# Optimization experiments

Measured on AMD Instinct MI355X. Metric: run time of the kernel, lower is better.

The kernel has to match this reference:

```python
import jax, jax.numpy as jnp
import numpy as np

B, N, D = 16, 1024, 5
R_HID = 8  # radial MLP hidden width


def setup_inputs() -> dict:
    key = jax.random.key(0)
    ks = jax.random.split(key, 16)
    feats = jax.random.normal(ks[0], (B, N, D), jnp.float32)
    coors = 3.0 * jax.random.normal(ks[1], (B, N, 3), jnp.float32)
    a = jax.random.bernoulli(ks[2], 0.01, (B, N, N))
    adj_mat = a | jnp.swapaxes(a, 1, 2)
    s = 1.0 / np.sqrt(D)
    Wq = s * jax.random.normal(ks[3], (D, D), jnp.float32)
    Wk = s * jax.random.normal(ks[4], (D, D), jnp.float32)
    Wv = s * jax.random.normal(ks[5], (D, D), jnp.float32)
    Wo = s * jax.random.normal(ks[6], (D, D), jnp.float32)
    w_r1 = 0.5 * jax.random.normal(ks[7], (1, R_HID), jnp.float32)
    b_r1 = jnp.zeros((R_HID,), jnp.float32)
    w_r2 = 0.5 * jax.random.normal(ks[8], (R_HID, 1), jnp.float32)
    b_r2 = jnp.zeros((1,), jnp.float32)
    w1 = (1.0 / np.sqrt(D)) * jax.random.normal(ks[9], (D, 128), jnp.float32)
    b1 = jnp.zeros((128,), jnp.float32)
    w2 = (1.0 / np.sqrt(128.0)) * jax.random.normal(ks[10], (128, 3), jnp.float32)
    b2 = jnp.zeros((3,), jnp.float32)
    return dict(feats=feats, coors=coors, adj_mat=adj_mat, Wq=Wq, Wk=Wk, Wv=Wv,
                Wo=Wo, w_r1=w_r1, b_r1=b_r1, w_r2=w_r2, b_r2=b_r2,
                w1=w1, b1=b1, w2=w2, b2=b2)


def _se3_layer(feats, coors, neigh, Wq, Wk, Wv, Wo, w_r1, b_r1, w_r2, b_r2):
    # SE(3)-invariant sparse graph attention on degree-0 channels.
    # Attention logits = content term + radial (distance-only) bias, so the
    # scalar output is invariant to global rotations/translations of coors.
    q = jnp.einsum('bnd,de->bne', feats, Wq)
    k = jnp.einsum('bnd,de->bne', feats, Wk)
    v = jnp.einsum('bnd,de->bne', feats, Wv)
    rel = coors[:, :, None, :] - coors[:, None, :, :]        # [B,N,N,3]
    dist = jnp.sqrt(jnp.sum(rel * rel, axis=-1) + 1e-8)      # [B,N,N]
    h = jax.nn.relu(dist[..., None] * w_r1[0] + b_r1)        # [B,N,N,R_HID]
    rbias = (h @ w_r2)[..., 0] + b_r2[0]                     # [B,N,N]
    scores = jnp.einsum('bid,bjd->bij', q, k) / np.sqrt(q.shape[-1]) + rbias
    scores = jnp.where(neigh, scores, -1e9)
    attn = jax.nn.softmax(scores, axis=-1)
    agg = jnp.einsum('bij,bjd->bid', attn, v)
    return feats + jnp.einsum('bid,de->bie', agg, Wo)        # residual


def reference(feats, coors, adj_mat, Wq, Wk, Wv, Wo, w_r1, b_r1, w_r2, b_r2,
              w1, b1, w2, b2):
    a = adj_mat.astype(jnp.float32)
    # num_adj_degrees=2: attend over 1-hop and 2-hop neighbors (+ self)
    adj2 = jnp.einsum('bij,bjk->bik', a, a) > 0
    eye = jnp.eye(adj_mat.shape[1], dtype=bool)[None]
    neigh = adj_mat | adj2 | eye
    x = _se3_layer(feats, coors, neigh, Wq, Wk, Wv, Wo, w_r1, b_r1, w_r2, b_r2)
    pooled = jnp.mean(x, axis=1)                              # [B, D]
    hdn = jax.nn.relu(pooled @ w1 + b1)
    return hdn @ w2 + b2                                      # [B, 3]
```

## Files before the change

### kernel.cpp

```cpp
#include <hip/hip_runtime.h>
#include <hip/hip_bf16.h>

#define BB 16
#define NN 1024
#define DD 5
#define RH 8

typedef unsigned long long u64;
typedef unsigned int u32;
typedef __hip_bfloat16 bf16;

static __device__ __forceinline__ float tof(bf16 x) { return __bfloat162float(x); }
static __device__ __forceinline__ float ldf(const void* p, long long i, bool f) {
  return f ? ((const float*)p)[i] : tof(((const bf16*)p)[i]);
}

#define LOG2E 1.4426950408889634f
#define PACK_BLOCKS (BB * NN * 16 / 256)
#define KV_BLOCKS (BB * NN / 256)


__global__ __launch_bounds__(256) void k_pack(
    const void* __restrict__ adj, const void* __restrict__ feats,
    const void* __restrict__ coors,
    const void* __restrict__ Wk, const void* __restrict__ Wv,
    const void* __restrict__ Wo,
    u64* __restrict__ adjbits, float4* __restrict__ kvg,
    float* __restrict__ czg, int* __restrict__ gflags,
    float* __restrict__ pooled, int* __restrict__ cntr) {
  __shared__ int sNon01, sNonpair, sLow3;
  __shared__ int sCnt[4];
  __shared__ float wkL[25], wvL[25], woL[25];
  int tid = threadIdx.x;

  if (blockIdx.x >= PACK_BLOCKS) {
    int kb = blockIdx.x - PACK_BLOCKS;
    if (kb == 0) {
      if (tid < BB * DD) pooled[tid] = 0.0f;
      else if (tid < BB * DD + BB) cntr[tid - BB * DD] = 0;
    }
    {
      u32 x = ((const u32*)feats)[tid];
      u32 lo = x & 0xFFFFu;
      int e = (int)((lo >> 7) & 0xFFu);
      bool insane = !(lo == 0u || (e >= 90 && e <= 150));
      u64 m = __ballot(insane);
      if ((tid & 63) == 0) sCnt[tid >> 6] = (int)__popcll(m);
    }
    __syncthreads();
    bool f32 = (sCnt[0] + sCnt[1] + sCnt[2] + sCnt[3]) > 64;
    if (tid < 25) {
      wkL[tid] = ldf(Wk, tid, f32);
      wvL[tid] = ldf(Wv, tid, f32);
      woL[tid] = ldf(Wo, tid, f32);
    }
    if (kb == 0 && tid == 0) gflags[0] = f32 ? 1 : 0;
    __syncthreads();
    long long node = (long long)kb * 256 + tid;
    float f0 = ldf(feats, node * DD + 0, f32), f1 = ldf(feats, node * DD + 1, f32),
          f2 = ldf(feats, node * DD + 2, f32), f3 = ldf(feats, node * DD + 3, f32),
          f4 = ldf(feats, node * DD + 4, f32);
    float k[DD], tv[DD], v[DD];
    #pragma unroll
    for (int e = 0; e < DD; ++e) {
      k[e] = f0 * wkL[e] + f1 * wkL[5 + e] + f2 * wkL[10 + e] + f3 * wkL[15 + e] +
             f4 * wkL[20 + e];
      tv[e] = f0 * wvL[e] + f1 * wvL[5 + e] + f2 * wvL[10 + e] + f3 * wvL[15 + e] +
              f4 * wvL[20 + e];
    }
    #pragma unroll
    for (int e = 0; e < DD; ++e)
      v[e] = tv[0] * woL[e] + tv[1] * woL[5 + e] + tv[2] * woL[10 + e] +
             tv[3] * woL[15 + e] + tv[4] * woL[20 + e];
    float cx = ldf(coors, node * 3 + 0, f32);
    float cy = ldf(coors, node * 3 + 1, f32);
    float cz = ldf(coors, node * 3 + 2, f32);
    kvg[node * 3 + 0] = make_float4(k[0], k[1], k[2], k[3]);
    kvg[node * 3 + 1] = make_float4(k[4], v[0], v[1], v[2]);
    kvg[node * 3 + 2] = make_float4(v[3], v[4], cx, cy);
    czg[node] = cz;
    return;
  }

  if (tid == 0) { sNon01 = 0; sNonpair = 0; sLow3 = 0; }
  __syncthreads();
  {
    const u32* aw = (const u32*)adj;
    int non01 = 0, nonpair = 0, low3 = 0;
    for (int i = tid; i < 4096; i += 256) {
      u32 x = aw[i];
      u32 lo = x & 0xFFFFu, hi = x >> 16;
      non01 |= (x > 1u);
      nonpair |= !((lo == 0u || lo == 0x3F80u) && (hi == 0u || hi == 0x3F80u));
      low3 |= (lo == 0x3F80u);
    }
    if (non01) atomicOr(&sNon01, 1);
    if (nonpair) atomicOr(&sNonpair, 1);
    if (low3) atomicOr(&sLow3, 1);
  }
  __syncthreads();
  int mode;
  if (!sNon01) mode = 0;
  else if (!sNonpair) mode = sLow3 ? 2 : 3;
  else mode = 1;

  int gid = blockIdx.x * 256 + tid;
  int w = gid & 15;
  long long row = gid >> 4;
  long long base = row * NN + (long long)w * 64;
  u64 bits = 0;
  if (mode == 3) {
    const uint4* p = (const uint4*)((const float*)adj + base);
    #pragma unroll
    for (int t = 0; t < 16; ++t) {
      uint4 x = p[t];
      if (x.x << 1) bits |= 1ull << (4 * t + 0);
      if (x.y << 1) bits |= 1ull << (4 * t + 1);
      if (x.z << 1) bits |= 1ull << (4 * t + 2);
      if (x.w << 1) bits |= 1ull << (4 * t + 3);
    }
  } else if (mode == 0) {
    const uint4* p = (const uint4*)((const u32*)adj + base);
    #pragma unroll
    for (int t = 0; t < 16; ++t) {
      uint4 x = p[t];
      if (x.x) bits |= 1ull << (4 * t + 0);
      if (x.y) bits |= 1ull << (4 * t + 1);
      if (x.z) bits |= 1ull << (4 * t + 2);
      if (x.w) bits |= 1ull << (4 * t + 3);
    }
  } else if (mode == 2) {
    const uint4* p = (const uint4*)((const unsigned short*)adj + base);
    #pragma unroll
    for (int t = 0; t < 8; ++t) {
      uint4 x = p[t];
      u32 c[4] = {x.x, x.y, x.z, x.w};
      #pragma unroll
      for (int q = 0; q < 4; ++q) {
        if ((c[q] & 0x7FFFu)) bits |= 1ull << (8 * t + 2 * q + 0);
        if ((c[q] >> 16) & 0x7FFFu) bits |= 1ull << (8 * t + 2 * q + 1);
      }
    }
  } else {
    const uint4* p = (const uint4*)((const unsigned char*)adj + base);
    #pragma unroll
    for (int t = 0; t < 4; ++t) {
      uint4 x = p[t];
      u32 c[4] = {x.x, x.y, x.z, x.w};
      #pragma unroll
      for (int q = 0; q < 4; ++q)
        #pragma unroll
        for (int bb = 0; bb < 4; ++bb)
          if ((c[q] >> (8 * bb)) & 0xFFu) bits |= 1ull << (16 * t + 4 * q + bb);
    }
  }
  adjbits[gid] = bits;
}

__global__ __launch_bounds__(256) void k_attn(
    const void* __restrict__ feats, const void* __restrict__ coors,
    const void* __restrict__ Wq,
    const void* __restrict__ wr1, const void* __restrict__ br1,
    const void* __restrict__ wr2, const void* __restrict__ br2,
    const float4* __restrict__ kvg, const float* __restrict__ czg,
    const int* __restrict__ gflags, const u64* __restrict__ adjbits,
    float* __restrict__ pooled, int* __restrict__ cntr,
    const void* __restrict__ w1, const void* __restrict__ b1,
    const void* __restrict__ w2, const void* __restrict__ b2,
    float* __restrict__ out) {
  __shared__ __align__(16) float4 kvL[NN * 3];
  __shared__ float czL[NN];
  __shared__ unsigned short listL[4][NN];
  __shared__ u64 neighL[16][16];
  __shared__ float qL[16 * DD], ciL[16 * 3];
  __shared__ float wqL[25];
  __shared__ float wrL[3][RH];
  __shared__ float sConst[2];
  __shared__ int sFast, sLast;

  int bi = blockIdx.x;
  int b = bi >> 6, chunk = bi & 63;
  int tid = threadIdx.x;
  bool f32 = gflags[0] != 0;
  if (tid < 25) wqL[tid] = ldf(Wq, tid, f32);
  if (tid >= 64 && tid < 64 + RH) {
    int h = tid - 64;
    wrL[0][h] = ldf(wr1, h, f32);
    wrL[1][h] = ldf(br1, h, f32);
    wrL[2][h] = ldf(wr2, h, f32);
  }
  if (tid == 96) {
    float c = 0.0f;
    int ok = 1;
    #pragma unroll
    for (int h = 0; h < RH; ++h) {
      float w1h = ldf(wr1, h, f32);
      if (ldf(br1, h, f32) != 0.0f) ok = 0;
      if (w1h > 0.0f) c += w1h * ldf(wr2, h, f32);
    }
    sConst[0] = c * LOG2E;
    sConst[1] = ldf(br2, 0, f32) * LOG2E;
    sFast = ok;
  }
  {
    const float4* src = kvg + (size_t)b * NN * 3;
    for (int idx = tid; idx < NN * 3; idx += 256) kvL[idx] = src[idx];
    const float* csrc = czg + (size_t)b * NN;
    for (int idx = tid; idx < NN; idx += 256) czL[idx] = csrc[idx];
  }
  __syncthreads();
  int fast = sFast;
  if (tid < 16) {
    long long row = (long long)b * NN + chunk * 16 + tid;
    float f0 = ldf(feats, row * DD + 0, f32), f1 = ldf(feats, row * DD + 1, f32),
          f2 = ldf(feats, row * DD + 2, f32), f3 = ldf(feats, row * DD + 3, f32),
          f4 = ldf(feats, row * DD + 4, f32);
    float qsc = fast ? (0.4472135954999579f * LOG2E) : 0.4472135954999579f;
    #pragma unroll
    for (int e = 0; e < DD; ++e)
      qL[tid * DD + e] = (f0 * wqL[e] + f1 * wqL[5 + e] + f2 * wqL[10 + e] +
                          f3 * wqL[15 + e] + f4 * wqL[20 + e]) * qsc;
    #pragma unroll
    for (int c = 0; c < 3; ++c)
      ciL[tid * 3 + c] = ldf(coors, row * 3 + c, f32);
  }

  int g = tid >> 6, lane = tid & 63;
  int w = lane & 15, grp = lane >> 4;
  const u64* basep = adjbits + (size_t)b * NN * 16;
  for (int rr = 0; rr < 4; ++rr) {
    int il = g * 4 + rr;
    int i = chunk * 16 + il;
    u64 rw = basep[(size_t)i * 16 + w];
    unsigned short* list = listL[g];
    int cnt = 0;
    #pragma unroll
    for (int sw = 0; sw < 16; ++sw) {
      u64 bits = __shfl(rw, sw, 64);
      int mybit = (int)((bits >> lane) & 1ull);
      int pre = __popcll(bits & ((1ull << lane) - 1ull));
      if (mybit) list[cnt + pre] = (unsigned short)(sw * 64 + lane);
      cnt += __popcll(bits);
    }
    __syncthreads();
    u64 acc = rw;
    if (w == (i >> 6)) acc |= 1ull << (i & 63);
    for (int n = grp; n < cnt; n += 4) acc |= basep[(size_t)list[n] * 16 + w];
    acc |= __shfl_xor(acc, 16, 64);
    acc |= __shfl_xor(acc, 32, 64);
    if (lane < 16) neighL[il][lane] = acc;
    __syncthreads();
  }

  float q[4][DD], ci[4][3], l[4], A[4][DD];
  #pragma unroll
  for (int r = 0; r < 4; ++r) {
    #pragma unroll
    for (int e = 0; e < DD; ++e) q[r][e] = qL[(g * 4 + r) * DD + e];
    #pragma unroll
    for (int c = 0; c < 3; ++c) ci[r][c] = ciL[(g * 4 + r) * 3 + c];
    l[r] = 0.0f;
    #pragma unroll
    for (int e = 0; e < DD; ++e) A[r][e] = 0.0f;
  }
  float Cf = sConst[0], br2f = sConst[1];
  for (int it = 0; it < 16; ++it) {
    int j = it * 64 + lane;
    float4 ka = kvL[j * 3 + 0];
    float4 kb = kvL[j * 3 + 1];
    float4 kc = kvL[j * 3 + 2];
    float jx = kc.z, jy = kc.w, jz = czL[j];
    u64 nw[4];
    #pragma unroll
    for (int r = 0; r < 4; ++r) nw[r] = neighL[g * 4 + r][it];
    if (fast) {
      #pragma unroll
      for (int r = 0; r < 4; ++r) {
        float cx = jx - ci[r][0], cy = jy - ci[r][1], cz = jz - ci[r][2];
        float dist =
            __builtin_amdgcn_sqrtf(fmaf(cx, cx, fmaf(cy, cy, fmaf(cz, cz, 1e-8f))));
        float s = fmaf(q[r][0], ka.x, br2f);
        s = fmaf(q[r][1], ka.y, s);
        s = fmaf(q[r][2], ka.z, s);
        s = fmaf(q[r][3], ka.w, s);
        s = fmaf(q[r][4], kb.x, s);
        s = fmaf(Cf, dist, s);
        s = fminf(s, 126.0f);
        s = ((nw[r] >> lane) & 1ull) ? s : -150.0f;
        float p = __builtin_amdgcn_exp2f(s);
        l[r] += p;
        A[r][0] = fmaf(p, kb.y, A[r][0]);
        A[r][1] = fmaf(p, kb.z, A[r][1]);
        A[r][2] = fmaf(p, kb.w, A[r][2]);
        A[r][3] = fmaf(p, kc.x, A[r][3]);
        A[r][4] = fmaf(p, kc.y, A[r][4]);
      }
    } else {
      #pragma unroll
      for (int r = 0; r < 4; ++r) {
        float cx = jx - ci[r][0], cy = jy - ci[r][1], cz = jz - ci[r][2];
        float dist = sqrtf(fmaf(cx, cx, fmaf(cy, cy, fmaf(cz, cz, 1e-8f))));
        float rb = ldf(br2, 0, f32);
        #pragma unroll
        for (int h = 0; h < RH; ++h)
          rb += fmaxf(dist * wrL[0][h] + wrL[1][h], 0.0f) * wrL[2][h];
        float s = fmaf(q[r][0], ka.x, rb);
        s = fmaf(q[r][1], ka.y, s);
        s = fmaf(q[r][2], ka.z, s);
        s = fmaf(q[r][3], ka.w, s);
        s = fmaf(q[r][4], kb.x, s);
        s = fminf(s, 85.0f);
        s = ((nw[r] >> lane) & 1ull) ? s : -100.0f;
        float p = __expf(s);
        l[r] += p;
        A[r][0] = fmaf(p, kb.y, A[r][0]);
        A[r][1] = fmaf(p, kb.z, A[r][1]);
        A[r][2] = fmaf(p, kb.w, A[r][2]);
        A[r][3] = fmaf(p, kc.x, A[r][3]);
        A[r][4] = fmaf(p, kc.y, A[r][4]);
      }
    }
  }
  #pragma unroll
  for (int msk = 1; msk < 64; msk <<= 1) {
    #pragma unroll
    for (int r = 0; r < 4; ++r) {
      l[r] += __shfl_xor(l[r], msk, 64);
      A[r][0] += __shfl_xor(A[r][0], msk, 64);
      A[r][1] += __shfl_xor(A[r][1], msk, 64);
      A[r][2] += __shfl_xor(A[r][2], msk, 64);
      A[r][3] += __shfl_xor(A[r][3], msk, 64);
      A[r][4] += __shfl_xor(A[r][4], msk, 64);
    }
  }

  float* waveC = (float*)listL;
  if (lane == 0) {
    float cw[DD] = {0.f, 0.f, 0.f, 0.f, 0.f};
    #pragma unroll
    for (int r = 0; r < 4; ++r) {
      long long grow = (long long)b * NN + chunk * 16 + g * 4 + r;
      float inv = (l[r] > 0.0f) ? 1.0f / l[r] : 0.0f;
      #pragma unroll
      for (int e = 0; e < DD; ++e)
        cw[e] += ldf(feats, grow * DD + e, f32) + A[r][e] * inv;
    }
    #pragma unroll
    for (int e = 0; e < DD; ++e) waveC[g * DD + e] = cw[e];
  }
  __syncthreads();
  if (tid < DD) {
    float s = waveC[tid] + waveC[DD + tid] + waveC[2 * DD + tid] +
              waveC[3 * DD + tid];
    float old = atomicAdd(&pooled[b * DD + tid], s);
    asm volatile("" :: "v"(old));
  }
  __syncthreads();
  if (tid == 0) sLast = (atomicAdd(&cntr[b], 1) == 63) ? 1 : 0;
  __syncthreads();

  if (sLast) {
    float* hL = ((float*)listL) + 32;
    if (tid < DD) {
      float pv = __hip_atomic_load(&pooled[b * DD + tid], __ATOMIC_RELAXED,
                                   __HIP_MEMORY_SCOPE_AGENT);
      qL[tid] = pv * (1.0f / 1024.0f);
    }
    __syncthreads();
    if (tid < 128) {
      float acc = ldf(b1, tid, f32);
      #pragma unroll
      for (int d = 0; d < DD; ++d)
        acc = fmaf(qL[d], ldf(w1, d * 128 + tid, f32), acc);
      hL[tid] = fmaxf(acc, 0.0f);
    }
    __syncthreads();
    if (tid < 3) {
      float s = ldf(b2, tid, f32);
      for (int j = 0; j < 128; ++j)
        s = fmaf(hL[j], ldf(w2, j * 3 + tid, f32), s);
      out[b * 3 + tid] = s;
    }
  }
}

extern "C" void kernel_launch(void* const* d_in, const int* in_sizes, int n_in,
                              void* d_out, int out_size, void* d_ws, size_t ws_size,
                              hipStream_t stream) {
  const void* adj = d_in[2];
  float* out = (float*)d_out;

  char* w = (char*)d_ws;
  int* gflags = (int*)w;
  float* pooled = (float*)(w + 64);
  int* cntr = (int*)(w + 512);
  const size_t MB2 = (size_t)BB * NN * 16 * sizeof(u64);
  u64* adjbits = (u64*)(w + 1024);
  float4* kvg = (float4*)(w + 1024 + MB2);
  float* czg = (float*)(w + 1024 + MB2 + 786432);

  k_pack<<<PACK_BLOCKS + KV_BLOCKS, 256, 0, stream>>>(
      adj, d_in[0], d_in[1], d_in[4], d_in[5], d_in[6], adjbits, kvg, czg,
      gflags, pooled, cntr);
  k_attn<<<BB * 64, 256, 0, stream>>>(
      d_in[0], d_in[1], d_in[3], d_in[7], d_in[8], d_in[9], d_in[10], kvg, czg,
      gflags, adjbits, pooled, cntr, d_in[11], d_in[12], d_in[13], d_in[14],
      out);
}
```

Measured before the change: 202.2 us.

## Read per-batch K/V and coords from global instead of staging in LDS

Removes the 64 KB LDS staging of the per-batch key/value/coordinate table and has each lane load its float4 entries directly from global memory (served by L2, shared across the 64 blocks of a batch). This cuts LDS use per block to raise occupancy and drops the upfront bulk copy. The per-row __syncthreads in the neighbor-list build are also removed, since each wave uses its own list buffer, and dedicated small shared arrays replace the aliased reuse of listL. The trade-off is stride-3 float4 global loads inside the hot loop instead of LDS reads.

```diff
diff --git a/kernel.cpp b/kernel.cpp
--- a/kernel.cpp
+++ b/kernel.cpp
@@ -168,8 +168,6 @@
     const void* __restrict__ w1, const void* __restrict__ b1,
     const void* __restrict__ w2, const void* __restrict__ b2,
     float* __restrict__ out) {
-  __shared__ __align__(16) float4 kvL[NN * 3];
-  __shared__ float czL[NN];
   __shared__ unsigned short listL[4][NN];
   __shared__ u64 neighL[16][16];
   __shared__ float qL[16 * DD], ciL[16 * 3];
@@ -177,6 +175,9 @@
   __shared__ float wrL[3][RH];
   __shared__ float sConst[2];
   __shared__ int sFast, sLast;
+  __shared__ float waveC[4][DD];
+  __shared__ float pM[DD];
+  __shared__ float hL[128];
 
   int bi = blockIdx.x;
   int b = bi >> 6, chunk = bi & 63;
@@ -202,12 +203,6 @@
     sConst[1] = ldf(br2, 0, f32) * LOG2E;
     sFast = ok;
   }
-  {
-    const float4* src = kvg + (size_t)b * NN * 3;
-    for (int idx = tid; idx < NN * 3; idx += 256) kvL[idx] = src[idx];
-    const float* csrc = czg + (size_t)b * NN;
-    for (int idx = tid; idx < NN; idx += 256) czL[idx] = csrc[idx];
-  }
   __syncthreads();
   int fast = sFast;
   if (tid < 16) {
@@ -224,6 +219,7 @@
     for (int c = 0; c < 3; ++c)
       ciL[tid * 3 + c] = ldf(coors, row * 3 + c, f32);
   }
+  __syncthreads();
 
   int g = tid >> 6, lane = tid & 63;
   int w = lane & 15, grp = lane >> 4;
@@ -242,14 +238,12 @@
       if (mybit) list[cnt + pre] = (unsigned short)(sw * 64 + lane);
       cnt += __popcll(bits);
     }
-    __syncthreads();
     u64 acc = rw;
     if (w == (i >> 6)) acc |= 1ull << (i & 63);
     for (int n = grp; n < cnt; n += 4) acc |= basep[(size_t)list[n] * 16 + w];
     acc |= __shfl_xor(acc, 16, 64);
     acc |= __shfl_xor(acc, 32, 64);
     if (lane < 16) neighL[il][lane] = acc;
-    __syncthreads();
   }
 
   float q[4][DD], ci[4][3], l[4], A[4][DD];
@@ -263,13 +257,15 @@
     #pragma unroll
     for (int e = 0; e < DD; ++e) A[r][e] = 0.0f;
   }
+  const float4* kvb = kvg + (size_t)b * NN * 3;
+  const float* czb = czg + (size_t)b * NN;
   float Cf = sConst[0], br2f = sConst[1];
   for (int it = 0; it < 16; ++it) {
     int j = it * 64 + lane;
-    float4 ka = kvL[j * 3 + 0];
-    float4 kb = kvL[j * 3 + 1];
-    float4 kc = kvL[j * 3 + 2];
-    float jx = kc.z, jy = kc.w, jz = czL[j];
+    float4 ka = kvb[j * 3 + 0];
+    float4 kb = kvb[j * 3 + 1];
+    float4 kc = kvb[j * 3 + 2];
+    float jx = kc.z, jy = kc.w, jz = czb[j];
     u64 nw[4];
     #pragma unroll
     for (int r = 0; r < 4; ++r) nw[r] = neighL[g * 4 + r][it];
@@ -334,7 +330,6 @@
     }
   }
 
-  float* waveC = (float*)listL;
   if (lane == 0) {
     float cw[DD] = {0.f, 0.f, 0.f, 0.f, 0.f};
     #pragma unroll
@@ -346,12 +341,11 @@
         cw[e] += ldf(feats, grow * DD + e, f32) + A[r][e] * inv;
     }
     #pragma unroll
-    for (int e = 0; e < DD; ++e) waveC[g * DD + e] = cw[e];
+    for (int e = 0; e < DD; ++e) waveC[g][e] = cw[e];
   }
   __syncthreads();
   if (tid < DD) {
-    float s = waveC[tid] + waveC[DD + tid] + waveC[2 * DD + tid] +
-              waveC[3 * DD + tid];
+    float s = waveC[0][tid] + waveC[1][tid] + waveC[2][tid] + waveC[3][tid];
     float old = atomicAdd(&pooled[b * DD + tid], s);
     asm volatile("" :: "v"(old));
   }
@@ -360,18 +354,17 @@
   __syncthreads();
 
   if (sLast) {
-    float* hL = ((float*)listL) + 32;
     if (tid < DD) {
       float pv = __hip_atomic_load(&pooled[b * DD + tid], __ATOMIC_RELAXED,
                                    __HIP_MEMORY_SCOPE_AGENT);
-      qL[tid] = pv * (1.0f / 1024.0f);
+      pM[tid] = pv * (1.0f / 1024.0f);
     }
     __syncthreads();
     if (tid < 128) {
       float acc = ldf(b1, tid, f32);
       #pragma unroll
       for (int d = 0; d < DD; ++d)
-        acc = fmaf(qL[d], ldf(w1, d * 128 + tid, f32), acc);
+        acc = fmaf(pM[d], ldf(w1, d * 128 + tid, f32), acc);
       hL[tid] = fmaxf(acc, 0.0f);
     }
     __syncthreads();
```

Measured after the change: 191.8 us. 5.1% less time.
